# Optimization experiments

Hardware: AMD Instinct MI355X
Metric: run time of the kernel (lower is better)

Reference implementation:

```python
import jax, jax.numpy as jnp
import numpy as np

B, N, E = 128, 256, 2048
BINS = 16

def _gcn(x, src, dst, W, b):
    # GCNConv with self-loops and symmetric deg^-1/2 normalization (PyG default).
    h = x @ W  # [N, Fout]
    deg = jnp.zeros(x.shape[0], x.dtype).at[dst].add(1.0) + 1.0  # +1 self-loop
    dinv = jax.lax.rsqrt(deg)
    coef = dinv[src] * dinv[dst]  # [E]
    agg = jnp.zeros_like(h).at[dst].add(h[src] * coef[:, None])
    return agg + h / deg[:, None] + b  # self-loop norm = 1/deg

def _gnn(x, ei, W1, b1, W2, b2, W3, b3):
    # x: [B,N,Fin], ei: [B,2,E]. Dropout skipped (eval mode).
    def single(x, ei):
        s, d = ei[0], ei[1]
        h = jax.nn.relu(_gcn(x, s, d, W1, b1))
        h = jax.nn.relu(_gcn(h, s, d, W2, b2))
        return _gcn(h, s, d, W3, b3)
    return jax.vmap(single)(x, ei)

def _att_pool(x, Watt):
    # SimGNN attention pooling; all graphs have exactly N nodes.
    ctx = jnp.tanh((x @ Watt.T).sum(axis=1) / jnp.asarray(N, x.dtype))  # [B,f3]
    scores = jax.nn.sigmoid(jnp.einsum('bnf,bf->bn', x, ctx))  # [B,N]
    return jnp.einsum('bnf,bn->bf', x, scores)  # [B,f3]

def _forward(xq, xc, eq, ec, W1, b1, W2, b2, W3, b3, Watt, ntnW, ntnV, ntnb, fc1W, fc1b, fc2W, fc2b):
    q = _gnn(xq, eq, W1, b1, W2, b2, W3, b3)  # [B,N,f3]
    c = _gnn(xc, ec, W1, b1, W2, b2, W3, b3)
    e1 = _att_pool(q, Watt)
    e2 = _att_pool(c, Watt)
    # NTN: bilinear + linear on concat + bias
    scores = jax.nn.relu(
        jnp.einsum('bi,tij,bj->bt', e1, ntnW, e2)
        + jnp.concatenate([e1, e2], axis=-1) @ ntnV.T
        + ntnb
    )  # [B, tensor_neurons]
    # histogram of all pairwise node-embedding dot products (torch.histc semantics)
    s = jnp.einsum('bnf,bmf->bnm', q, c).ravel()
    lo, hi = s.min(), s.max()
    idx = jnp.clip(jnp.floor((s - lo) / (hi - lo) * BINS).astype(jnp.int32), 0, BINS - 1)
    counts = jnp.zeros(BINS, s.dtype).at[idx].add(1.0)
    h = jax.lax.stop_gradient(counts / counts.sum())
    scores = jnp.concatenate([scores, jnp.broadcast_to(h, (scores.shape[0], BINS))], axis=1)
    scores = jax.nn.relu(scores @ fc1W.T + fc1b)
    p = jax.nn.sigmoid(scores @ fc2W.T + fc2b)  # [B,1]
    return p.squeeze()


def setup_inputs() -> dict:
    key = jax.random.key(0)
    ks = jax.random.split(key, 20)
    Fin, f1, f2, f3, T, BN = 128, 128, 64, 32, 16, 16
    def xav(k, shape):
        fan_in, fan_out = shape[-1], shape[0]
        lim = np.sqrt(6.0 / (fan_in + fan_out))
        return jax.random.uniform(k, shape, jnp.float32, -lim, lim)
    return {
        'xq': jax.random.normal(ks[0], (B, N, Fin), jnp.float32),
        'xc': jax.random.normal(ks[1], (B, N, Fin), jnp.float32),
        'eq': jax.random.randint(ks[2], (B, 2, E), 0, N, jnp.int32),
        'ec': jax.random.randint(ks[3], (B, 2, E), 0, N, jnp.int32),
        'W1': xav(ks[4], (Fin, f1)), 'b1': jnp.zeros((f1,), jnp.float32),
        'W2': xav(ks[5], (f1, f2)), 'b2': jnp.zeros((f2,), jnp.float32),
        'W3': xav(ks[6], (f2, f3)), 'b3': jnp.zeros((f3,), jnp.float32),
        'Watt': xav(ks[7], (f3, f3)),
        'ntnW': xav(ks[8], (T, f3, f3)),
        'ntnV': xav(ks[9], (T, 2 * f3)),
        'ntnb': xav(ks[10], (T, 1)).squeeze(-1),
        'fc1W': xav(ks[11], (BN, T + BINS)), 'fc1b': jnp.zeros((BN,), jnp.float32),
        'fc2W': xav(ks[12], (1, BN)), 'fc2b': jnp.zeros((1,), jnp.float32),
    }


def reference(xq, xc, eq, ec, W1, b1, W2, b2, W3, b3, Watt, ntnW, ntnV, ntnb, fc1W, fc1b, fc2W, fc2b):
    return _forward(xq, xc, eq, ec, W1, b1, W2, b2, W3, b3, Watt, ntnW, ntnV, ntnb, fc1W, fc1b, fc2W, fc2b)
```

## Files before the change

### kernel.cpp

```cpp
#include <hip/hip_runtime.h>
#include <math.h>

#define BB 128
#define NN 256
#define EE 2048
#define BINS 16

typedef unsigned short u16;

__global__ void csr_kernel(const int* __restrict__ eq, const int* __restrict__ ec,
                           int* __restrict__ off, u16* __restrict__ srcs,
                           float* __restrict__ wts) {
    int g = blockIdx.x;
    int b = g < BB ? g : g - BB;
    const int* ei = g < BB ? eq : ec;
    int t = threadIdx.x;
    __shared__ int cnt[NN];
    __shared__ int sa[NN], sb[NN];
    __shared__ int cursor[NN];
    __shared__ float dvs[NN];
    cnt[t] = 0;
    __syncthreads();
    const int* src = ei + b * 2 * EE;
    const int* dst = src + EE;
    for (int e = t; e < EE; e += 256) atomicAdd(&cnt[dst[e]], 1);
    __syncthreads();
    dvs[t] = rsqrtf((float)cnt[t] + 1.0f);
    sa[t] = cnt[t];
    __syncthreads();
    int* pin = sa; int* pout = sb;
    for (int d = 1; d < NN; d <<= 1) {
        int v = pin[t];
        if (t >= d) v += pin[t - d];
        pout[t] = v;
        __syncthreads();
        int* tmp = pin; pin = pout; pout = tmp;
    }
    int excl = pin[t] - cnt[t];
    off[g * 257 + t] = excl;
    if (t == 255) off[g * 257 + 256] = EE;
    cursor[t] = excl;
    __syncthreads();
    for (int e = t; e < EE; e += 256) {
        int d = dst[e], s = src[e];
        int pos = atomicAdd(&cursor[d], 1);
        srcs[g * EE + pos] = (u16)s;
        wts[g * EE + pos] = dvs[s] * dvs[d];
    }
}

template<int FIN, int FOUT, bool RELU, int NSPLIT>
__global__ __launch_bounds__(512) void gcn_fused6(
        const float* __restrict__ X0, const float* __restrict__ X1,
        const float* __restrict__ W, const float* __restrict__ bias,
        const int* __restrict__ off, const u16* __restrict__ srcs,
        const float* __restrict__ wts, float* __restrict__ OUT) {
    constexpr int CHUNKS = FOUT / 32;
    constexpr int NW = FIN / 16;
    constexpr int BUF = 16 * 260 + 16 * 32;
    int blk = blockIdx.x;
    int g = blk % (2 * BB);
    int rest = blk / (2 * BB);
    int cb = (rest % CHUNKS) * 32;
    int half = rest / CHUNKS;
    int t = threadIdx.x;

    __shared__ float uni[2 * BUF];
    __shared__ int   eoff[NN + 1];
    __shared__ u16   esrc[EE];
    __shared__ float ewt[EE];
    float* hT = uni;

    const float* xg = (g < BB) ? (X0 + (size_t)g * NN * FIN)
                               : (X1 + (size_t)(g - BB) * NN * FIN);
    const int* o = off + g * 257;
    const u16* sr = srcs + (size_t)g * EE;
    const float* wg = wts + (size_t)g * EE;

    for (int i = t; i < EE; i += 512) { esrc[i] = sr[i]; ewt[i] = wg[i]; }
    for (int i = t; i <= NN; i += 512) eoff[i] = o[i];

    int l = t & 63;
    int wv = t >> 6;

    float acc[4][4];
#pragma unroll
    for (int i = 0; i < 4; i++)
#pragma unroll
        for (int j = 0; j < 4; j++) acc[i][j] = 0.f;

    int sn = t >> 1, qk = (t & 1) * 8;
    const float* xr = xg + sn * FIN + qk;
    int wrow = t >> 5, wcol = t & 31;

    auto stage = [&](float* buf, const float4& s0, const float4& s1, float sw) {
        buf[(qk + 0) * 260 + sn] = s0.x;
        buf[(qk + 1) * 260 + sn] = s0.y;
        buf[(qk + 2) * 260 + sn] = s0.z;
        buf[(qk + 3) * 260 + sn] = s0.w;
        buf[(qk + 4) * 260 + sn] = s1.x;
        buf[(qk + 5) * 260 + sn] = s1.y;
        buf[(qk + 6) * 260 + sn] = s1.z;
        buf[(qk + 7) * 260 + sn] = s1.w;
        buf[16 * 260 + t] = sw;
    };

    float4 rA0 = *(const float4*)(xr);
    float4 rA1 = *(const float4*)(xr + 4);
    float  wA  = W[(size_t)wrow * FOUT + cb + wcol];
    float4 rB0 = *(const float4*)(xr + 16);
    float4 rB1 = *(const float4*)(xr + 20);
    float  wB  = W[(size_t)(16 + wrow) * FOUT + cb + wcol];
    stage(uni, rA0, rA1, wA);
    if (NW > 2) {
        rA0 = *(const float4*)(xr + 32);
        rA1 = *(const float4*)(xr + 36);
        wA  = W[(size_t)(32 + wrow) * FOUT + cb + wcol];
    }
    __syncthreads();

#pragma unroll
    for (int it = 0; it < NW; ++it) {
        float* cur = uni + (it & 1) * BUF;
        if (it + 1 < NW) {
            float* nb = uni + ((it + 1) & 1) * BUF;
            if (((it + 1) & 1) == 0) stage(nb, rA0, rA1, wA);
            else                     stage(nb, rB0, rB1, wB);
            if (it + 3 < NW) {
                int ko = (it + 3) * 16;
                if (((it + 3) & 1) == 0) {
                    rA0 = *(const float4*)(xr + ko);
                    rA1 = *(const float4*)(xr + ko + 4);
                    wA  = W[(size_t)(ko + wrow) * FOUT + cb + wcol];
                } else {
                    rB0 = *(const float4*)(xr + ko);
                    rB1 = *(const float4*)(xr + ko + 4);
                    wB  = W[(size_t)(ko + wrow) * FOUT + cb + wcol];
                }
            }
        }
#pragma unroll
        for (int k = 0; k < 16; k++) {
            float4 xv  = *(const float4*)&cur[k * 260 + 4 * l];
            float4 wvv = *(const float4*)&cur[16 * 260 + k * 32 + 4 * wv];
            acc[0][0] += xv.x * wvv.x; acc[0][1] += xv.x * wvv.y;
            acc[0][2] += xv.x * wvv.z; acc[0][3] += xv.x * wvv.w;
            acc[1][0] += xv.y * wvv.x; acc[1][1] += xv.y * wvv.y;
            acc[1][2] += xv.y * wvv.z; acc[1][3] += xv.y * wvv.w;
            acc[2][0] += xv.z * wvv.x; acc[2][1] += xv.z * wvv.y;
            acc[2][2] += xv.z * wvv.z; acc[2][3] += xv.z * wvv.w;
            acc[3][0] += xv.w * wvv.x; acc[3][1] += xv.w * wvv.y;
            acc[3][2] += xv.w * wvv.z; acc[3][3] += xv.w * wvv.w;
        }
        __syncthreads();
    }
#pragma unroll
    for (int i = 0; i < 4; i++)
#pragma unroll
        for (int j = 0; j < 4; j++)
            hT[(4 * l + i) * 33 + 4 * wv + j] = acc[i][j];
    __syncthreads();

    int c = t & 31, ng = t >> 5;
    float bb_ = bias[cb + c];
    float* outp = OUT + (size_t)g * NN * FOUT;
    constexpr int NSEG = NN / NSPLIT;
    int nlo = half * NSEG, nhi = nlo + NSEG;
    for (int n = nlo + ng; n < nhi; n += 16) {
        int j0 = eoff[n], j1 = eoff[n + 1];
        float a = 0.f;
        int j = j0;
        for (; j + 1 < j1; j += 2) {
            int s0 = esrc[j], s1 = esrc[j + 1];
            a += hT[s0 * 33 + c] * ewt[j];
            a += hT[s1 * 33 + c] * ewt[j + 1];
        }
        if (j < j1) {
            a += hT[esrc[j] * 33 + c] * ewt[j];
        }
        float d0i = 1.0f / ((float)(j1 - j0) + 1.0f);
        float val = a + hT[n * 33 + c] * d0i + bb_;
        if (RELU) val = fmaxf(val, 0.f);
        outp[n * FOUT + cb + c] = val;
    }
}

__global__ void attpool_kernel(const float* __restrict__ X, const float* __restrict__ Watt,
                               float* __restrict__ e) {
    int g = blockIdx.x;
    int t = threadIdx.x;
    __shared__ float xs[NN * 33];
    __shared__ float red[256];
    __shared__ float mean_s[32], ctx_s[32], sc[NN];
    const float* x = X + (size_t)g * NN * 32;
    for (int i = t; i < NN * 32; i += 256) { int n = i >> 5, c = i & 31; xs[n * 33 + c] = x[i]; }
    __syncthreads();
    {
        int c = t & 31, p = t >> 5;
        float s = 0.f;
        for (int n = p * 32; n < (p + 1) * 32; n++) s += xs[n * 33 + c];
        red[t] = s;
    }
    __syncthreads();
    if (t < 32) {
        float m = 0.f;
        for (int p = 0; p < 8; p++) m += red[p * 32 + t];
        mean_s[t] = m / (float)NN;
    }
    __syncthreads();
    if (t < 32) {
        float a = 0.f;
        for (int f = 0; f < 32; f++) a += mean_s[f] * Watt[t * 32 + f];
        ctx_s[t] = tanhf(a);
    }
    __syncthreads();
    {
        float a = 0.f;
        for (int f = 0; f < 32; f++) a += xs[t * 33 + f] * ctx_s[f];
        sc[t] = 1.f / (1.f + expf(-a));
    }
    __syncthreads();
    {
        int c = t & 31, p = t >> 5;
        float s = 0.f;
        for (int n = p * 32; n < (p + 1) * 32; n++) s += xs[n * 33 + c] * sc[n];
        red[t] = s;
    }
    __syncthreads();
    if (t < 32) {
        float s = 0.f;
        for (int p = 0; p < 8; p++) s += red[p * 32 + t];
        e[g * 32 + t] = s;
    }
}

#define PD_STAGE_AND_DOT \
    int blk = blockIdx.x; \
    int b = blk >> 2; \
    int tq = (blk >> 1) & 1, tc = blk & 1; \
    __shared__ float qsT[32 * 132]; \
    __shared__ float csT[32 * 132]; \
    int t = threadIdx.x; \
    { \
        int n = t >> 1, f0 = (t & 1) * 16; \
        const float* qp = Q + ((size_t)b * NN + tq * 128 + n) * 32 + f0; \
        const float* cp = C + ((size_t)b * NN + tc * 128 + n) * 32 + f0; \
        float qa16[16], ca16[16]; \
        *(float4*)&qa16[0]  = *(const float4*)(qp); \
        *(float4*)&qa16[4]  = *(const float4*)(qp + 4); \
        *(float4*)&qa16[8]  = *(const float4*)(qp + 8); \
        *(float4*)&qa16[12] = *(const float4*)(qp + 12); \
        *(float4*)&ca16[0]  = *(const float4*)(cp); \
        *(float4*)&ca16[4]  = *(const float4*)(cp + 4); \
        *(float4*)&ca16[8]  = *(const float4*)(cp + 8); \
        *(float4*)&ca16[12] = *(const float4*)(cp + 12); \
        _Pragma("unroll") \
        for (int m = 0; m < 16; m++) { \
            qsT[(f0 + m) * 132 + n] = qa16[m]; \
            csT[(f0 + m) * 132 + n] = ca16[m]; \
        } \
    } \
    __syncthreads(); \
    int rg = (t >> 4) * 4, cg = (t & 15) * 4; \
    float acc[8][8]; \
    _Pragma("unroll") \
    for (int i = 0; i < 8; i++) \
        _Pragma("unroll") \
        for (int j = 0; j < 8; j++) acc[i][j] = 0.f; \
    _Pragma("unroll 2") \
    for (int f = 0; f < 32; f++) { \
        float4 qa = *(const float4*)&qsT[f * 132 + rg]; \
        float4 qb = *(const float4*)&qsT[f * 132 + 64 + rg]; \
        float4 ca = *(const float4*)&csT[f * 132 + cg]; \
        float4 cb = *(const float4*)&csT[f * 132 + 64 + cg]; \
        float qv[8] = {qa.x, qa.y, qa.z, qa.w, qb.x, qb.y, qb.z, qb.w}; \
        float cv[8] = {ca.x, ca.y, ca.z, ca.w, cb.x, cb.y, cb.z, cb.w}; \
        _Pragma("unroll") \
        for (int i = 0; i < 8; i++) \
            _Pragma("unroll") \
            for (int j = 0; j < 8; j++) acc[i][j] += qv[i] * cv[j]; \
    }

__global__ __launch_bounds__(256, 4) void pairdot_minmax(
        const float* __restrict__ Q, const float* __restrict__ C,
        float* __restrict__ bmin, float* __restrict__ bmax) {
    PD_STAGE_AND_DOT
    float lmin = acc[0][0], lmax = acc[0][0];
#pragma unroll
    for (int i = 0; i < 8; i++)
#pragma unroll
        for (int j = 0; j < 8; j++) {
            lmin = fminf(lmin, acc[i][j]);
            lmax = fmaxf(lmax, acc[i][j]);
        }
    __shared__ float rmin[256], rmax[256];
    rmin[t] = lmin; rmax[t] = lmax;
    __syncthreads();
    for (int s = 128; s > 0; s >>= 1) {
        if (t < s) { rmin[t] = fminf(rmin[t], rmin[t + s]); rmax[t] = fmaxf(rmax[t], rmax[t + s]); }
        __syncthreads();
    }
    if (t == 0) { bmin[blk] = rmin[0]; bmax[blk] = rmax[0]; }
}

__global__ void minmax_kernel(const float* __restrict__ bmin, const float* __restrict__ bmax,
                              float* __restrict__ lohi, float* __restrict__ counts) {
    __shared__ float rmin[256], rmax[256];
    int t = threadIdx.x;
    float lmin = 1e30f, lmax = -1e30f;
    for (int i = t; i < 512; i += 256) { lmin = fminf(lmin, bmin[i]); lmax = fmaxf(lmax, bmax[i]); }
    rmin[t] = lmin; rmax[t] = lmax;
    __syncthreads();
    for (int s = 128; s > 0; s >>= 1) {
        if (t < s) { rmin[t] = fminf(rmin[t], rmin[t + s]); rmax[t] = fmaxf(rmax[t], rmax[t + s]); }
        __syncthreads();
    }
    if (t == 0) { lohi[0] = rmin[0]; lohi[1] = rmax[0]; }
    if (t < BINS) counts[t] = 0.f;
}

__global__ __launch_bounds__(256, 4) void pairdot_hist(
        const float* __restrict__ Q, const float* __restrict__ C,
        const float* __restrict__ lohi, float* __restrict__ counts) {
    PD_STAGE_AND_DOT
    float lo = lohi[0], hi = lohi[1];
    float scale = (float)BINS / (hi - lo);
    int lane = t & 63;
    int cnt = 0;
#pragma unroll
    for (int i = 0; i < 8; i++)
#pragma unroll
        for (int j = 0; j < 8; j++) {
            int idx = (int)floorf((acc[i][j] - lo) * scale);
            idx = min(max(idx, 0), BINS - 1);
            unsigned long long b0 = __ballot((idx & 1) != 0);
            unsigned long long b1 = __ballot((idx & 2) != 0);
            unsigned long long b2 = __ballot((idx & 4) != 0);
            unsigned long long b3 = __ballot((idx & 8) != 0);
            unsigned long long msk = ((lane & 1) ? b0 : ~b0);
            msk &= ((lane & 2) ? b1 : ~b1);
            msk &= ((lane & 4) ? b2 : ~b2);
            msk &= ((lane & 8) ? b3 : ~b3);
            cnt += __popcll(msk);
        }
    __shared__ float wbins[4][BINS];
    int wave = t >> 6;
    if (lane < BINS) wbins[wave][lane] = (float)cnt;
    __syncthreads();
    if (t < BINS) {
        atomicAdd(&counts[t], wbins[0][t] + wbins[1][t] + wbins[2][t] + wbins[3][t]);
    }
}

__global__ void final_kernel(const float* __restrict__ e1, const float* __restrict__ e2,
                             const float* __restrict__ ntnW, const float* __restrict__ ntnV,
                             const float* __restrict__ ntnb, const float* __restrict__ counts,
                             const float* __restrict__ fc1W, const float* __restrict__ fc1b,
                             const float* __restrict__ fc2W, const float* __restrict__ fc2b,
                             float* __restrict__ out) {
    int b = blockIdx.x;
    int t = threadIdx.x;
    __shared__ float a1[32], a2[32], red[256], z[32], u[16];
    if (t < 32) a1[t] = e1[b * 32 + t];
    else if (t < 64) a2[t - 32] = e2[b * 32 + t - 32];
    __syncthreads();
    int tt = t >> 4, g = t & 15;
    float p = 0.f;
#pragma unroll
    for (int ii = 0; ii < 2; ii++) {
        int i = g + 16 * ii;
        float d = 0.f;
        const float* wr = ntnW + (tt * 32 + i) * 32;
        for (int j = 0; j < 32; j++) d += wr[j] * a2[j];
        p += a1[i] * d;
    }
    red[t] = p;
    __syncthreads();
    if (t < 16) {
        float s = 0.f;
        for (int g2 = 0; g2 < 16; g2++) s += red[t * 16 + g2];
        float lin = ntnb[t];
        for (int i = 0; i < 32; i++) lin += ntnV[t * 64 + i] * a1[i];
        for (int i = 0; i < 32; i++) lin += ntnV[t * 64 + 32 + i] * a2[i];
        z[t] = fmaxf(s + lin, 0.f);
    } else if (t < 32) {
        float tot = 0.f;
        for (int i = 0; i < BINS; i++) tot += counts[i];
        z[t] = counts[t - 16] / tot;
    }
    __syncthreads();
    if (t < 16) {
        float a = fc1b[t];
        for (int i = 0; i < 32; i++) a += fc1W[t * 32 + i] * z[i];
        u[t] = fmaxf(a, 0.f);
    }
    __syncthreads();
    if (t == 0) {
        float a = fc2b[0];
        for (int i = 0; i < 16; i++) a += fc2W[i] * u[i];
        out[b] = 1.f / (1.f + expf(-a));
    }
}

extern "C" void kernel_launch(void* const* d_in, const int* in_sizes, int n_in,
                              void* d_out, int out_size, void* d_ws, size_t ws_size,
                              hipStream_t stream) {
    const float* xq   = (const float*)d_in[0];
    const float* xc   = (const float*)d_in[1];
    const int*   eq   = (const int*)d_in[2];
    const int*   ec   = (const int*)d_in[3];
    const float* W1   = (const float*)d_in[4];
    const float* b1   = (const float*)d_in[5];
    const float* W2   = (const float*)d_in[6];
    const float* b2   = (const float*)d_in[7];
    const float* W3   = (const float*)d_in[8];
    const float* b3   = (const float*)d_in[9];
    const float* Watt = (const float*)d_in[10];
    const float* ntnW = (const float*)d_in[11];
    const float* ntnV = (const float*)d_in[12];
    const float* ntnb = (const float*)d_in[13];
    const float* fc1W = (const float*)d_in[14];
    const float* fc1b = (const float*)d_in[15];
    const float* fc2W = (const float*)d_in[16];
    const float* fc2b = (const float*)d_in[17];
    float* out = (float*)d_out;
    float* ws  = (float*)d_ws;

    float* O3   = ws;
    float* e12  = O3 + 2097152;
    float* bmin = e12 + 8192;
    float* bmax = bmin + 2048;
    float* lohi = bmax + 2048;
    float* cntw = lohi + 2;
    int*   off  = (int*)(ws + 2109504);
    u16*   srcs = (u16*)(off + 65792);
    float* wts  = ws + 2437440;
    float* O1   = ws + 3223872;
    float* O2   = O1 + 8388608;

    float* O3Q = O3;
    float* O3C = O3 + (size_t)BB * NN * 32;
    float* e1w = e12;
    float* e2w = e12 + BB * 32;

    csr_kernel<<<2 * BB, 256, 0, stream>>>(eq, ec, off, srcs, wts);

    gcn_fused6<128, 128, true, 1><<<4 * 2 * BB, 512, 0, stream>>>(
        xq, xc, W1, b1, off, srcs, wts, O1);
    gcn_fused6<128, 64, true, 1><<<2 * 2 * BB, 512, 0, stream>>>(
        O1, O1 + (size_t)BB * NN * 128, W2, b2, off, srcs, wts, O2);
    gcn_fused6<64, 32, false, 2><<<2 * 2 * BB, 512, 0, stream>>>(
        O2, O2 + (size_t)BB * NN * 64, W3, b3, off, srcs, wts, O3);

    attpool_kernel<<<2 * BB, 256, 0, stream>>>(O3, Watt, e12);

    pairdot_minmax<<<BB * 4, 256, 0, stream>>>(O3Q, O3C, bmin, bmax);
    minmax_kernel<<<1, 256, 0, stream>>>(bmin, bmax, lohi, cntw);
    pairdot_hist<<<BB * 4, 256, 0, stream>>>(O3Q, O3C, lohi, cntw);

    final_kernel<<<BB, 256, 0, stream>>>(e1w, e2w, ntnW, ntnV, ntnb, cntw,
                                         fc1W, fc1b, fc2W, fc2b, out);
}
```

Measured before the change: 299.6 us.

## Preload full weight slice to LDS and use single-buffered 32-wide X tiles

The GCN GEMM stage now loads the whole W column slice for the block into shared memory once, instead of streaming one row of W per 16-wide K step. X is staged through a single 32-wide transposed buffer with register prefetch, replacing the 16-wide double buffer. This halves the number of K-step barriers and removes the per-step W global loads. In exchange it uses more LDS per block (W slice plus a larger union buffer), which may reduce occupancy, and the single X buffer adds a barrier between compute and each refill.

```diff
diff --git a/kernel.cpp b/kernel.cpp
--- a/kernel.cpp
+++ b/kernel.cpp
@@ -50,14 +50,14 @@
 }
 
 template<int FIN, int FOUT, bool RELU, int NSPLIT>
-__global__ __launch_bounds__(512) void gcn_fused6(
+__global__ __launch_bounds__(512) void gcn_fused7(
         const float* __restrict__ X0, const float* __restrict__ X1,
         const float* __restrict__ W, const float* __restrict__ bias,
         const int* __restrict__ off, const u16* __restrict__ srcs,
         const float* __restrict__ wts, float* __restrict__ OUT) {
     constexpr int CHUNKS = FOUT / 32;
-    constexpr int NW = FIN / 16;
-    constexpr int BUF = 16 * 260 + 16 * 32;
+    constexpr int NT = FIN / 32;
+    constexpr int UNI = (32 * 260 > NN * 33) ? 32 * 260 : NN * 33;
     int blk = blockIdx.x;
     int g = blk % (2 * BB);
     int rest = blk / (2 * BB);
@@ -65,84 +65,61 @@
     int half = rest / CHUNKS;
     int t = threadIdx.x;
 
-    __shared__ float uni[2 * BUF];
+    __shared__ float uni[UNI];
+    __shared__ float Ws[FIN * 32];
     __shared__ int   eoff[NN + 1];
     __shared__ u16   esrc[EE];
     __shared__ float ewt[EE];
+    float* Xs = uni;
     float* hT = uni;
 
     const float* xg = (g < BB) ? (X0 + (size_t)g * NN * FIN)
                                : (X1 + (size_t)(g - BB) * NN * FIN);
-    const int* o = off + g * 257;
-    const u16* sr = srcs + (size_t)g * EE;
-    const float* wg = wts + (size_t)g * EE;
-
-    for (int i = t; i < EE; i += 512) { esrc[i] = sr[i]; ewt[i] = wg[i]; }
-    for (int i = t; i <= NN; i += 512) eoff[i] = o[i];
+
+    {
+        const int* o = off + g * 257;
+        const u16* sre = srcs + (size_t)g * EE;
+        const float* wge = wts + (size_t)g * EE;
+        for (int i = t; i < EE; i += 512) { esrc[i] = sre[i]; ewt[i] = wge[i]; }
+        for (int i = t; i <= NN; i += 512) eoff[i] = o[i];
+    }
+#pragma unroll
+    for (int j = 0; j < FIN * 32 / 2048; ++j) {
+        int i = (t + 512 * j) * 4;
+        int k = i >> 5, c = i & 31;
+        *(float4*)&Ws[i] = *(const float4*)&W[(size_t)k * FOUT + cb + c];
+    }
+
+    int r = t >> 1, q = (t & 1) * 16;
+    const float* xrow = xg + (size_t)r * FIN;
+    float4 px[4];
+
+#define LOADPX(k0) { _Pragma("unroll") \
+    for (int j = 0; j < 4; ++j) px[j] = *(const float4*)(xrow + (k0) + q + 4 * j); }
+#define WRITEPX() { _Pragma("unroll") \
+    for (int j = 0; j < 4; ++j) { float4 v = px[j]; int m = q + 4 * j; \
+        Xs[(m + 0) * 260 + r] = v.x; Xs[(m + 1) * 260 + r] = v.y; \
+        Xs[(m + 2) * 260 + r] = v.z; Xs[(m + 3) * 260 + r] = v.w; } }
 
     int l = t & 63;
     int wv = t >> 6;
-
     float acc[4][4];
 #pragma unroll
     for (int i = 0; i < 4; i++)
 #pragma unroll
         for (int j = 0; j < 4; j++) acc[i][j] = 0.f;
 
-    int sn = t >> 1, qk = (t & 1) * 8;
-    const float* xr = xg + sn * FIN + qk;
-    int wrow = t >> 5, wcol = t & 31;
-
-    auto stage = [&](float* buf, const float4& s0, const float4& s1, float sw) {
-        buf[(qk + 0) * 260 + sn] = s0.x;
-        buf[(qk + 1) * 260 + sn] = s0.y;
-        buf[(qk + 2) * 260 + sn] = s0.z;
-        buf[(qk + 3) * 260 + sn] = s0.w;
-        buf[(qk + 4) * 260 + sn] = s1.x;
-        buf[(qk + 5) * 260 + sn] = s1.y;
-        buf[(qk + 6) * 260 + sn] = s1.z;
-        buf[(qk + 7) * 260 + sn] = s1.w;
-        buf[16 * 260 + t] = sw;
-    };
-
-    float4 rA0 = *(const float4*)(xr);
-    float4 rA1 = *(const float4*)(xr + 4);
-    float  wA  = W[(size_t)wrow * FOUT + cb + wcol];
-    float4 rB0 = *(const float4*)(xr + 16);
-    float4 rB1 = *(const float4*)(xr + 20);
-    float  wB  = W[(size_t)(16 + wrow) * FOUT + cb + wcol];
-    stage(uni, rA0, rA1, wA);
-    if (NW > 2) {
-        rA0 = *(const float4*)(xr + 32);
-        rA1 = *(const float4*)(xr + 36);
-        wA  = W[(size_t)(32 + wrow) * FOUT + cb + wcol];
-    }
-    __syncthreads();
-
-#pragma unroll
-    for (int it = 0; it < NW; ++it) {
-        float* cur = uni + (it & 1) * BUF;
-        if (it + 1 < NW) {
-            float* nb = uni + ((it + 1) & 1) * BUF;
-            if (((it + 1) & 1) == 0) stage(nb, rA0, rA1, wA);
-            else                     stage(nb, rB0, rB1, wB);
-            if (it + 3 < NW) {
-                int ko = (it + 3) * 16;
-                if (((it + 3) & 1) == 0) {
-                    rA0 = *(const float4*)(xr + ko);
-                    rA1 = *(const float4*)(xr + ko + 4);
-                    wA  = W[(size_t)(ko + wrow) * FOUT + cb + wcol];
-                } else {
-                    rB0 = *(const float4*)(xr + ko);
-                    rB1 = *(const float4*)(xr + ko + 4);
-                    wB  = W[(size_t)(ko + wrow) * FOUT + cb + wcol];
-                }
-            }
-        }
-#pragma unroll
-        for (int k = 0; k < 16; k++) {
-            float4 xv  = *(const float4*)&cur[k * 260 + 4 * l];
-            float4 wvv = *(const float4*)&cur[16 * 260 + k * 32 + 4 * wv];
+    LOADPX(0);
+    WRITEPX();
+    if (NT > 1) LOADPX(32);
+    __syncthreads();
+
+#pragma unroll
+    for (int tile = 0; tile < NT; ++tile) {
+#pragma unroll
+        for (int kk = 0; kk < 32; ++kk) {
+            float4 xv  = *(const float4*)&Xs[kk * 260 + 4 * l];
+            float4 wvv = *(const float4*)&Ws[(tile * 32 + kk) * 32 + 4 * wv];
             acc[0][0] += xv.x * wvv.x; acc[0][1] += xv.x * wvv.y;
             acc[0][2] += xv.x * wvv.z; acc[0][3] += xv.x * wvv.w;
             acc[1][0] += xv.y * wvv.x; acc[1][1] += xv.y * wvv.y;
@@ -153,6 +130,11 @@
             acc[3][2] += xv.w * wvv.z; acc[3][3] += xv.w * wvv.w;
         }
         __syncthreads();
+        if (tile + 1 < NT) {
+            WRITEPX();
+            if (tile + 2 < NT) LOADPX((tile + 2) * 32);
+            __syncthreads();
+        }
     }
 #pragma unroll
     for (int i = 0; i < 4; i++)
@@ -175,14 +157,14 @@
             a += hT[s0 * 33 + c] * ewt[j];
             a += hT[s1 * 33 + c] * ewt[j + 1];
         }
-        if (j < j1) {
-            a += hT[esrc[j] * 33 + c] * ewt[j];
-        }
+        if (j < j1) a += hT[esrc[j] * 33 + c] * ewt[j];
         float d0i = 1.0f / ((float)(j1 - j0) + 1.0f);
         float val = a + hT[n * 33 + c] * d0i + bb_;
         if (RELU) val = fmaxf(val, 0.f);
         outp[n * FOUT + cb + c] = val;
     }
+#undef LOADPX
+#undef WRITEPX
 }
 
 __global__ void attpool_kernel(const float* __restrict__ X, const float* __restrict__ Watt,
@@ -445,11 +427,11 @@
 
     csr_kernel<<<2 * BB, 256, 0, stream>>>(eq, ec, off, srcs, wts);
 
-    gcn_fused6<128, 128, true, 1><<<4 * 2 * BB, 512, 0, stream>>>(
+    gcn_fused7<128, 128, true, 1><<<4 * 2 * BB, 512, 0, stream>>>(
         xq, xc, W1, b1, off, srcs, wts, O1);
-    gcn_fused6<128, 64, true, 1><<<2 * 2 * BB, 512, 0, stream>>>(
+    gcn_fused7<128, 64, true, 1><<<2 * 2 * BB, 512, 0, stream>>>(
         O1, O1 + (size_t)BB * NN * 128, W2, b2, off, srcs, wts, O2);
-    gcn_fused6<64, 32, false, 2><<<2 * 2 * BB, 512, 0, stream>>>(
+    gcn_fused7<64, 32, false, 2><<<2 * 2 * BB, 512, 0, stream>>>(
         O2, O2 + (size_t)BB * NN * 64, W3, b3, off, srcs, wts, O3);
 
     attpool_kernel<<<2 * BB, 256, 0, stream>>>(O3, Watt, e12);
```

After: 333.6 us. +11.3%, slower.
